# Kernel tuning notes

Measured on AMD Instinct MI355X. Metric: run time of the kernel, lower is better.

The kernel has to match this reference:

```python
import jax, jax.numpy as jnp
import numpy as np

M0, M1 = 16, 16          # n_modes
C = 64                   # hidden_channels
B = 16                   # batch
H = W = 128              # spatial resolution
SCALE = C ** (-2)        # matches torch: scale * torch.rand(...)


def setup_inputs() -> dict:
    key = jax.random.key(0)
    kx, k0r, k0i, k1r, k1i = jax.random.split(key, 5)
    X = jax.random.normal(kx, (B, C, H, W), dtype=jnp.float32)
    wshape = (C, C, M0, M1)
    # torch.rand with cfloat draws U[0,1) for real and imag parts independently
    w0r = SCALE * jax.random.uniform(k0r, wshape, dtype=jnp.float32)
    w0i = SCALE * jax.random.uniform(k0i, wshape, dtype=jnp.float32)
    w1r = SCALE * jax.random.uniform(k1r, wshape, dtype=jnp.float32)
    w1i = SCALE * jax.random.uniform(k1i, wshape, dtype=jnp.float32)
    return {"X": X, "w0r": w0r, "w0i": w0i, "w1r": w1r, "w1i": w1i}


def reference(X, w0r, w0i, w1r, w1i):
    w0 = w0r + 1j * w0i                       # linear0: (C, C, M0, M1) complex
    w1 = w1r + 1j * w1i                       # linear1
    Xf = jnp.fft.rfftn(X, axes=(-2, -1), norm="forward")   # (B, C, H, W//2+1) complex
    # out[b,c] = sum_t weight[c,t] * Xf[b,t] on the two kept-mode corners
    top = jnp.einsum("ctxy,btxy->bcxy", w0, Xf[:, :, :M0, :M1])
    bot = jnp.einsum("ctxy,btxy->bcxy", w1, Xf[:, :, -M0:, :M1])
    Y = jnp.zeros_like(Xf)
    Y = Y.at[:, :, :M0, :M1].set(top)
    Y = Y.at[:, :, -M0:, :M1].set(bot)
    out = jnp.fft.irfftn(Y, axes=(-2, -1), s=(H, W), norm="forward")
    return out.astype(jnp.float32)
```

## Files before the change

kernel.cpp:

```cpp
#include <hip/hip_runtime.h>

#define PI2 6.28318530717958647692f

__global__ __launch_bounds__(256, 4) void k_fwd(const float* __restrict__ X,
                                                float* __restrict__ Xf) {
  __shared__ __attribute__((aligned(16))) float A2t[17 * 134 * 2];
  __shared__ __attribute__((aligned(16))) float Xc[4][8 * 128];
  const int plane = blockIdx.x;
  const int tid = threadIdx.x;
  const float* Xp = X + (size_t)plane * (128 * 128);

  {
    const int w2 = tid & 63;
    const int kxq = tid >> 6;
    const int lrow = tid >> 5;
    const int col = (tid & 31) * 4;

    float Wr[4], Wi[4], Tr[4], Ti[4];
    #pragma unroll
    for (int j = 0; j < 4; ++j) {
      int s = kxq * 4 + j;
      int kx = (s == 0) ? 16 : s;
      __sincosf(-PI2 * (float)kx / 128.f, &Wi[j], &Wr[j]);
      Tr[j] = 1.f; Ti[j] = 0.f;
    }
    float ar[4][2], ai[4][2];
    #pragma unroll
    for (int j = 0; j < 4; ++j) {
      ar[j][0] = 0.f; ar[j][1] = 0.f; ai[j][0] = 0.f; ai[j][1] = 0.f;
    }
    float dc0 = 0.f, dc1 = 0.f;

    {
      float4 v0, v1, v2;
      int r0g = (lrow < 4) ? lrow : (60 + lrow);
      int r1g = (lrow < 4) ? (4 + lrow) : (64 + lrow);
      int r2g = (lrow < 4) ? (8 + lrow) : (68 + lrow);
      v0 = *(const float4*)&Xp[r0g * 128 + col];
      v1 = *(const float4*)&Xp[r1g * 128 + col];
      v2 = *(const float4*)&Xp[r2g * 128 + col];
      *(float4*)&Xc[0][lrow * 128 + col] = v0;
      *(float4*)&Xc[1][lrow * 128 + col] = v1;
      *(float4*)&Xc[2][lrow * 128 + col] = v2;
    }
    __syncthreads();

    for (int c = 0; c < 16; ++c) {
      float4 nv;
      if (c < 13) {
        int rg = (lrow < 4) ? (4 * (c + 3) + lrow)
                            : (60 + 4 * (c + 3) + lrow);
        nv = *(const float4*)&Xp[rg * 128 + col];
      }
      const float* Xb = &Xc[c & 3][0];
      #pragma unroll
      for (int jj = 0; jj < 4; ++jj) {
        float2 tt = *(const float2*)&Xb[jj * 128 + 2 * w2];
        float2 bb = *(const float2*)&Xb[(jj + 4) * 128 + 2 * w2];
        float uex = tt.x + bb.x, uox = tt.x - bb.x;
        float uey = tt.y + bb.y, uoy = tt.y - bb.y;
        ar[0][0] = fmaf(uex, Tr[0], ar[0][0]); ai[0][0] = fmaf(uex, Ti[0], ai[0][0]);
        ar[0][1] = fmaf(uey, Tr[0], ar[0][1]); ai[0][1] = fmaf(uey, Ti[0], ai[0][1]);
        ar[1][0] = fmaf(uox, Tr[1], ar[1][0]); ai[1][0] = fmaf(uox, Ti[1], ai[1][0]);
        ar[1][1] = fmaf(uoy, Tr[1], ar[1][1]); ai[1][1] = fmaf(uoy, Ti[1], ai[1][1]);
        ar[2][0] = fmaf(uex, Tr[2], ar[2][0]); ai[2][0] = fmaf(uex, Ti[2], ai[2][0]);
        ar[2][1] = fmaf(uey, Tr[2], ar[2][1]); ai[2][1] = fmaf(uey, Ti[2], ai[2][1]);
        ar[3][0] = fmaf(uox, Tr[3], ar[3][0]); ai[3][0] = fmaf(uox, Ti[3], ai[3][0]);
        ar[3][1] = fmaf(uoy, Tr[3], ar[3][1]); ai[3][1] = fmaf(uoy, Ti[3], ai[3][1]);
        if (kxq == 0) { dc0 += uex; dc1 += uey; }
        #pragma unroll
        for (int j = 0; j < 4; ++j) {
          float nr = Tr[j] * Wr[j] - Ti[j] * Wi[j];
          float ni = Tr[j] * Wi[j] + Ti[j] * Wr[j];
          Tr[j] = nr; Ti[j] = ni;
        }
      }
      if (c == 7) {
        Tr[0] = 1.f;  Ti[0] = 0.f;
        Tr[1] = 0.f;  Ti[1] = -1.f;
        Tr[2] = -1.f; Ti[2] = 0.f;
        Tr[3] = 0.f;  Ti[3] = 1.f;
      }
      if (c < 13)
        *(float4*)&Xc[(c + 3) & 3][lrow * 128 + col] = nv;
      __syncthreads();
    }

    #pragma unroll
    for (int j = 0; j < 4; ++j) {
      int s = kxq * 4 + j;
      int row = (s == 0) ? 16 : s;
      *(float4*)&A2t[(row * 134 + 2 * w2) * 2] =
          make_float4(ar[j][0], ai[j][0], ar[j][1], ai[j][1]);
    }
    if (kxq == 0) {
      *(float4*)&A2t[(2 * w2) * 2] = make_float4(dc0, 0.f, dc1, 0.f);
    }
  }
  __syncthreads();

  {
    const int kxi = tid >> 3;
    const int t = tid & 7;
    const int row = (kxi < 16) ? kxi : (32 - kxi);
    const float csign = (kxi < 16) ? 1.f : -1.f;
    const float s = (t & 1) ? -1.f : 1.f;
    float s0r, s0i, s1r, s1i;
    __sincosf(-PI2 * (float)t / 128.f, &s0i, &s0r);
    __sincosf(-PI2 * (float)(t + 8) / 128.f, &s1i, &s1r);
    float r0 = 0.f, i0 = 0.f, r1 = 0.f, i1 = 0.f;
    float E0r = 1.f, E0i = 0.f, E1r = 1.f, E1i = 0.f;
    #pragma unroll
    for (int half = 0; half < 2; ++half) {
      if (half == 1) {
        float c_, s_;
        __sincosf(-1.57079632679489662f * (float)t, &s_, &c_);
        E0r = c_; E0i = s_; E1r = c_; E1i = s_;
      }
      #pragma unroll 4
      for (int w = half * 32; w < half * 32 + 32; ++w) {
        float2 a = *(const float2*)&A2t[(row * 134 + w) * 2];
        float2 b = *(const float2*)&A2t[(row * 134 + w + 64) * 2];
        float ur = fmaf(s, b.x, a.x);
        float ui = csign * fmaf(s, b.y, a.y);
        r0 = fmaf(ur, E0r, r0); r0 = fmaf(-ui, E0i, r0);
        i0 = fmaf(ur, E0i, i0); i0 = fmaf(ui, E0r, i0);
        r1 = fmaf(ur, E1r, r1); r1 = fmaf(-ui, E1i, r1);
        i1 = fmaf(ur, E1i, i1); i1 = fmaf(ui, E1r, i1);
        float u0 = E0r * s0r - E0i * s0i; E0i = E0r * s0i + E0i * s0r; E0r = u0;
        float u1 = E1r * s1r - E1i * s1i; E1i = E1r * s1i + E1i * s1r; E1r = u1;
      }
    }
    const float sc = 1.f / 16384.f;
    float* base = Xf + (size_t)plane * 1024 + kxi * 32;
    *(float2*)&base[t * 2]       = make_float2(r0 * sc, i0 * sc);
    *(float2*)&base[(t + 8) * 2] = make_float2(r1 * sc, i1 * sc);
  }
}

__global__ __launch_bounds__(256, 2) void k_mix(const float* __restrict__ Xf,
                                                const float* __restrict__ w0r,
                                                const float* __restrict__ w0i,
                                                const float* __restrict__ w1r,
                                                const float* __restrict__ w1i,
                                                float* __restrict__ Y) {
  __shared__ __attribute__((aligned(16))) float Wl[4 * 32 * 16 * 4];
  const int bid = blockIdx.x;
  const int c2 = bid >> 8;
  const int x  = (bid >> 4) & 15;
  const int cg = bid & 15;
  const int c0 = cg * 4;
  const int kxi = c2 * 16 + x;
  const float* Wr_g = c2 ? w1r : w0r;
  const float* Wi_g = c2 ? w1i : w0i;
  const int tid = threadIdx.x;
  const int b = tid >> 4;
  const int y = tid & 15;

  #pragma unroll
  for (int k = 0; k < 16; ++k) {
    int idx = tid + k * 256;
    int y_ = idx & 15, t_ = (idx >> 4) & 63, c_ = idx >> 10;
    size_t ga = (((size_t)(c0 + c_) * 64 + t_) * 16 + x) * 16 + y_;
    int f2i = ((c_ * 32 + (t_ >> 1)) * 16 + y_) * 2 + (t_ & 1);
    *(float2*)&Wl[f2i * 2] = make_float2(Wr_g[ga], Wi_g[ga]);
  }
  __syncthreads();

  float aR[4] = {}, aI[4] = {};
  const float* xbase = Xf + ((size_t)b * 64) * 1024 + kxi * 32 + y * 2;
  for (int t8 = 0; t8 < 64; t8 += 8) {
    float2 xv[8];
    #pragma unroll
    for (int q = 0; q < 8; ++q)
      xv[q] = *(const float2*)&xbase[(size_t)(t8 + q) * 1024];
    #pragma unroll
    for (int p = 0; p < 4; ++p) {
      int t2 = (t8 >> 1) + p;
      float2 xe = xv[2 * p], xo = xv[2 * p + 1];
      #pragma unroll
      for (int cj = 0; cj < 4; ++cj) {
        float4 wv = *(const float4*)&Wl[((cj * 32 + t2) * 16 + y) * 4];
        aR[cj] = fmaf(xe.x, wv.x, aR[cj]); aR[cj] = fmaf(-xe.y, wv.y, aR[cj]);
        aI[cj] = fmaf(xe.x, wv.y, aI[cj]); aI[cj] = fmaf(xe.y, wv.x, aI[cj]);
        aR[cj] = fmaf(xo.x, wv.z, aR[cj]); aR[cj] = fmaf(-xo.y, wv.w, aR[cj]);
        aI[cj] = fmaf(xo.x, wv.w, aI[cj]); aI[cj] = fmaf(xo.y, wv.z, aI[cj]);
      }
    }
  }
  #pragma unroll
  for (int cj = 0; cj < 4; ++cj) {
    size_t ya = ((size_t)(b * 64 + c0 + cj)) * 1024 + kxi * 32 + y * 2;
    *(float2*)&Y[ya] = make_float2(aR[cj], aI[cj]);
  }
}

__global__ __launch_bounds__(256, 4) void k_inv(const float* __restrict__ Y,
                                                float* __restrict__ out) {
  __shared__ __attribute__((aligned(16))) float Yl[1024];
  __shared__ __attribute__((aligned(16))) float Mt[128 * 16 * 2];
  const int plane = blockIdx.x;
  const int tid = threadIdx.x;
  *(float4*)&Yl[tid * 4] = *(const float4*)&Y[(size_t)plane * 1024 + tid * 4];
  __syncthreads();

  {
    const int g = tid >> 6;
    const int h2 = tid & 63;
    float zr[2][4] = {}, zi[2][4] = {};
    float uw, uwi;
    __sincosf(PI2 * (float)h2 / 128.f, &uwi, &uw);
    const float4* Yl4 = (const float4*)Yl;
    float Tr = 1.f, Ti = 0.f;
    #pragma unroll 4
    for (int kxi = 0; kxi < 16; ++kxi) {
      float sgn = (kxi & 1) ? -1.f : 1.f;
      #pragma unroll
      for (int q = 0; q < 2; ++q) {
        float4 p = Yl4[kxi * 8 + g * 2 + q];
        float cr0 = p.x * Tr - p.y * Ti, ci0 = p.x * Ti + p.y * Tr;
        float cr1 = p.z * Tr - p.w * Ti, ci1 = p.z * Ti + p.w * Tr;
        zr[0][2*q]   += cr0; zi[0][2*q]   += ci0;
        zr[0][2*q+1] += cr1; zi[0][2*q+1] += ci1;
        zr[1][2*q]   = fmaf(sgn, cr0, zr[1][2*q]);   zi[1][2*q]   = fmaf(sgn, ci0, zi[1][2*q]);
        zr[1][2*q+1] = fmaf(sgn, cr1, zr[1][2*q+1]); zi[1][2*q+1] = fmaf(sgn, ci1, zi[1][2*q+1]);
      }
      float nr = Tr * uw - Ti * uwi, ni = Tr * uwi + Ti * uw;
      Tr = nr; Ti = ni;
    }
    __sincosf(PI2 * (float)((112 * h2) & 127) / 128.f, &Ti, &Tr);
    #pragma unroll 4
    for (int kxi = 16; kxi < 32; ++kxi) {
      float sgn = (kxi & 1) ? -1.f : 1.f;
      #pragma unroll
      for (int q = 0; q < 2; ++q) {
        float4 p = Yl4[kxi * 8 + g * 2 + q];
        float cr0 = p.x * Tr - p.y * Ti, ci0 = p.x * Ti + p.y * Tr;
        float cr1 = p.z * Tr - p.w * Ti, ci1 = p.z * Ti + p.w * Tr;
        zr[0][2*q]   += cr0; zi[0][2*q]   += ci0;
        zr[0][2*q+1] += cr1; zi[0][2*q+1] += ci1;
        zr[1][2*q]   = fmaf(sgn, cr0, zr[1][2*q]);   zi[1][2*q]   = fmaf(sgn, ci0, zi[1][2*q]);
        zr[1][2*q+1] = fmaf(sgn, cr1, zr[1][2*q+1]); zi[1][2*q+1] = fmaf(sgn, ci1, zi[1][2*q+1]);
      }
      float nr = Tr * uw - Ti * uwi, ni = Tr * uwi + Ti * uw;
      Tr = nr; Ti = ni;
    }
    #pragma unroll
    for (int hs = 0; hs < 2; ++hs) {
      int h = h2 + hs * 64;
      #pragma unroll
      for (int q = 0; q < 2; ++q) {
        int ky0 = g * 4 + 2 * q;
        float f0 = (ky0 == 0) ? 1.f : 2.f;
        float4 v = make_float4(f0 * zr[hs][2*q],   -f0 * zi[hs][2*q],
                               2.f * zr[hs][2*q+1], -2.f * zi[hs][2*q+1]);
        int f4i = h * 8 + ((g * 2 + q) ^ (h & 7));
        *(float4*)&Mt[f4i * 4] = v;
      }
    }
  }
  __syncthreads();

  {
    const int hp = tid >> 5;
    const int w2 = tid & 31;
    float C[16], S[16];
    {
      float cw, sw;
      __sincosf(PI2 * (float)w2 / 128.f, &sw, &cw);
      C[0] = 1.f; S[0] = 0.f;
      #pragma unroll
      for (int k = 1; k < 16; ++k) {
        C[k] = C[k - 1] * cw - S[k - 1] * sw;
        S[k] = C[k - 1] * sw + S[k - 1] * cw;
      }
    }
    float* op = out + (size_t)plane * (128 * 128);
    const float4* Mt4 = (const float4*)Mt;
    #pragma unroll 4
    for (int hj = 0; hj < 16; ++hj) {
      int h = hp * 16 + hj;
      float e = 0.f, o = 0.f, e2 = 0.f, o2 = 0.f;
      #pragma unroll
      for (int j = 0; j < 8; ++j) {
        float4 m = Mt4[h * 8 + (j ^ (h & 7))];
        int k0 = 2 * j, k1 = 2 * j + 1;
        e = fmaf(m.x, C[k0], e); e = fmaf(m.y, S[k0], e);
        o = fmaf(m.z, C[k1], o); o = fmaf(m.w, S[k1], o);
        if ((k0 & 2) == 0) { e2 = fmaf(m.x, C[k0], e2); e2 = fmaf(m.y, S[k0], e2); }
        else               { e2 = fmaf(-m.x, C[k0], e2); e2 = fmaf(-m.y, S[k0], e2); }
        if ((k1 & 2) == 0) { o2 = fmaf(m.w, C[k1], o2); o2 = fmaf(-m.z, S[k1], o2); }
        else               { o2 = fmaf(-m.w, C[k1], o2); o2 = fmaf(m.z, S[k1], o2); }
      }
      op[h * 128 + w2]      = e + o;
      op[h * 128 + w2 + 64] = e - o;
      op[h * 128 + w2 + 32] = e2 + o2;
      op[h * 128 + w2 + 96] = e2 - o2;
    }
  }
}

extern "C" void kernel_launch(void* const* d_in, const int* in_sizes, int n_in,
                              void* d_out, int out_size, void* d_ws, size_t ws_size,
                              hipStream_t stream) {
  const float* X   = (const float*)d_in[0];
  const float* w0r = (const float*)d_in[1];
  const float* w0i = (const float*)d_in[2];
  const float* w1r = (const float*)d_in[3];
  const float* w1i = (const float*)d_in[4];
  float* outp = (float*)d_out;
  float* Xf = (float*)d_ws;
  float* Yw = (float*)d_ws + (1u << 20);
  k_fwd<<<1024, 256, 0, stream>>>(X, Xf);
  k_mix<<<512, 256, 0, stream>>>(Xf, w0r, w0i, w1r, w1i, Yw);
  k_inv<<<1024, 256, 0, stream>>>(Yw, outp);
}
```

Baseline: 169.6 us.

## Fuse spectral channel mixing into the inverse transform kernel

```diff
diff --git a/kernel.cpp b/kernel.cpp
--- a/kernel.cpp
+++ b/kernel.cpp
@@ -138,70 +138,43 @@
   }
 }
 
-__global__ __launch_bounds__(256, 2) void k_mix(const float* __restrict__ Xf,
-                                                const float* __restrict__ w0r,
-                                                const float* __restrict__ w0i,
-                                                const float* __restrict__ w1r,
-                                                const float* __restrict__ w1i,
-                                                float* __restrict__ Y) {
-  __shared__ __attribute__((aligned(16))) float Wl[4 * 32 * 16 * 4];
-  const int bid = blockIdx.x;
-  const int c2 = bid >> 8;
-  const int x  = (bid >> 4) & 15;
-  const int cg = bid & 15;
-  const int c0 = cg * 4;
-  const int kxi = c2 * 16 + x;
-  const float* Wr_g = c2 ? w1r : w0r;
-  const float* Wi_g = c2 ? w1i : w0i;
-  const int tid = threadIdx.x;
-  const int b = tid >> 4;
-  const int y = tid & 15;
-
-  #pragma unroll
-  for (int k = 0; k < 16; ++k) {
-    int idx = tid + k * 256;
-    int y_ = idx & 15, t_ = (idx >> 4) & 63, c_ = idx >> 10;
-    size_t ga = (((size_t)(c0 + c_) * 64 + t_) * 16 + x) * 16 + y_;
-    int f2i = ((c_ * 32 + (t_ >> 1)) * 16 + y_) * 2 + (t_ & 1);
-    *(float2*)&Wl[f2i * 2] = make_float2(Wr_g[ga], Wi_g[ga]);
-  }
-  __syncthreads();
-
-  float aR[4] = {}, aI[4] = {};
-  const float* xbase = Xf + ((size_t)b * 64) * 1024 + kxi * 32 + y * 2;
-  for (int t8 = 0; t8 < 64; t8 += 8) {
-    float2 xv[8];
-    #pragma unroll
-    for (int q = 0; q < 8; ++q)
-      xv[q] = *(const float2*)&xbase[(size_t)(t8 + q) * 1024];
-    #pragma unroll
-    for (int p = 0; p < 4; ++p) {
-      int t2 = (t8 >> 1) + p;
-      float2 xe = xv[2 * p], xo = xv[2 * p + 1];
-      #pragma unroll
-      for (int cj = 0; cj < 4; ++cj) {
-        float4 wv = *(const float4*)&Wl[((cj * 32 + t2) * 16 + y) * 4];
-        aR[cj] = fmaf(xe.x, wv.x, aR[cj]); aR[cj] = fmaf(-xe.y, wv.y, aR[cj]);
-        aI[cj] = fmaf(xe.x, wv.y, aI[cj]); aI[cj] = fmaf(xe.y, wv.x, aI[cj]);
-        aR[cj] = fmaf(xo.x, wv.z, aR[cj]); aR[cj] = fmaf(-xo.y, wv.w, aR[cj]);
-        aI[cj] = fmaf(xo.x, wv.w, aI[cj]); aI[cj] = fmaf(xo.y, wv.z, aI[cj]);
-      }
-    }
-  }
-  #pragma unroll
-  for (int cj = 0; cj < 4; ++cj) {
-    size_t ya = ((size_t)(b * 64 + c0 + cj)) * 1024 + kxi * 32 + y * 2;
-    *(float2*)&Y[ya] = make_float2(aR[cj], aI[cj]);
-  }
-}
-
-__global__ __launch_bounds__(256, 4) void k_inv(const float* __restrict__ Y,
-                                                float* __restrict__ out) {
+__global__ __launch_bounds__(256, 4) void k_mixinv(const float* __restrict__ Xf,
+                                                   const float* __restrict__ w0r,
+                                                   const float* __restrict__ w0i,
+                                                   const float* __restrict__ w1r,
+                                                   const float* __restrict__ w1i,
+                                                   float* __restrict__ out) {
   __shared__ __attribute__((aligned(16))) float Yl[1024];
   __shared__ __attribute__((aligned(16))) float Mt[128 * 16 * 2];
-  const int plane = blockIdx.x;
+  const int bid = blockIdx.x;
+  const int b = bid >> 6;
+  const int c = bid & 63;
   const int tid = threadIdx.x;
-  *(float4*)&Yl[tid * 4] = *(const float4*)&Y[(size_t)plane * 1024 + tid * 4];
+
+  {
+    const int m0 = 2 * tid;
+    const int kxi = m0 >> 4;
+    const int ky = m0 & 15;
+    const int x = (kxi < 16) ? kxi : (kxi - 16);
+    const float* Wr = (kxi < 16) ? w0r : w1r;
+    const float* Wi = (kxi < 16) ? w0i : w1i;
+    const float* xfp = Xf + ((size_t)b * 64) * 1024 + tid * 4;
+    const size_t woff = ((size_t)c * 64 * 16 + x) * 16 + ky;
+    const float* wrp = Wr + woff;
+    const float* wip = Wi + woff;
+    float yR0 = 0.f, yI0 = 0.f, yR1 = 0.f, yI1 = 0.f;
+    #pragma unroll 4
+    for (int t = 0; t < 64; ++t) {
+      float4 xf = *(const float4*)&xfp[(size_t)t * 1024];
+      float2 wr = *(const float2*)&wrp[t * 256];
+      float2 wi = *(const float2*)&wip[t * 256];
+      yR0 = fmaf(xf.x, wr.x, yR0); yR0 = fmaf(-xf.y, wi.x, yR0);
+      yI0 = fmaf(xf.x, wi.x, yI0); yI0 = fmaf(xf.y, wr.x, yI0);
+      yR1 = fmaf(xf.z, wr.y, yR1); yR1 = fmaf(-xf.w, wi.y, yR1);
+      yI1 = fmaf(xf.z, wi.y, yI1); yI1 = fmaf(xf.w, wr.y, yI1);
+    }
+    *(float4*)&Yl[tid * 4] = make_float4(yR0, yI0, yR1, yI1);
+  }
   __syncthreads();
 
   {
@@ -275,7 +248,7 @@
         S[k] = C[k - 1] * sw + S[k - 1] * cw;
       }
     }
-    float* op = out + (size_t)plane * (128 * 128);
+    float* op = out + (size_t)bid * (128 * 128);
     const float4* Mt4 = (const float4*)Mt;
     #pragma unroll 4
     for (int hj = 0; hj < 16; ++hj) {
@@ -310,8 +283,6 @@
   const float* w1i = (const float*)d_in[4];
   float* outp = (float*)d_out;
   float* Xf = (float*)d_ws;
-  float* Yw = (float*)d_ws + (1u << 20);
   k_fwd<<<1024, 256, 0, stream>>>(X, Xf);
-  k_mix<<<512, 256, 0, stream>>>(Xf, w0r, w0i, w1r, w1i, Yw);
-  k_inv<<<1024, 256, 0, stream>>>(Yw, outp);
+  k_mixinv<<<1024, 256, 0, stream>>>(Xf, w0r, w0i, w1r, w1i, outp);
 }
```

Result: slower. 179.5 us (+5.9%).
